# Kernel tuning notes

Measured on AMD Instinct MI355X. Metric: run time of the kernel, lower is better.

Reference implementation:

```python
import jax, jax.numpy as jnp
import numpy as np

D_MODEL = 1024
N_HEADS = 16
HEAD_DIM = 64
INNER = N_HEADS * HEAD_DIM
D_FF = 4096


def ln_novar(x, w, b):
    # mean-only 'layernorm' (no variance division), per original LayerNormNoVar
    u = jnp.mean(x, axis=-1, keepdims=True)
    return w * (x - u) + b


def setup_inputs() -> dict:
    key = jax.random.key(0)
    ks = jax.random.split(key, 12)
    s = lambda k, shape, scale: jax.random.normal(k, shape, dtype=jnp.float32) * scale
    inp = {
        "src": s(ks[0], (4, 2048, D_MODEL), 1.0),
        "pre_norm_w": jnp.ones((D_MODEL,), jnp.float32),
        "pre_norm_b": jnp.zeros((D_MODEL,), jnp.float32),
        "wq": s(ks[1], (D_MODEL, INNER), 0.02),
        "wk": s(ks[2], (D_MODEL, INNER), 0.02),
        "wv": s(ks[3], (D_MODEL, INNER), 0.02),
        "w_proj": s(ks[4], (INNER, D_MODEL), 0.02),
        "b_proj": jnp.zeros((D_MODEL,), jnp.float32),
        "norm1_w": jnp.ones((D_MODEL,), jnp.float32),
        "norm1_b": jnp.zeros((D_MODEL,), jnp.float32),
        "w1": s(ks[5], (D_MODEL, D_FF), 0.02),
        "b1": jnp.zeros((D_FF,), jnp.float32),
        "w2": s(ks[6], (D_FF, D_MODEL), 0.02),
        "b2": jnp.zeros((D_MODEL,), jnp.float32),
    }
    return inp


def reference(src, pre_norm_w, pre_norm_b, wq, wk, wv, w_proj, b_proj,
              norm1_w, norm1_b, w1, b1, w2, b2):
    B, N, _ = src.shape
    scale = HEAD_DIM ** -0.5
    x = ln_novar(src, pre_norm_w, pre_norm_b)
    q = (x @ wq).reshape(B, N, N_HEADS, HEAD_DIM)
    k = (x @ wk).reshape(B, N, N_HEADS, HEAD_DIM)
    v = (x @ wv).reshape(B, N, N_HEADS, HEAD_DIM)
    attn = jnp.einsum('bqhd,bkhd->bhqk', q, k) * scale
    attn = jax.nn.softmax(attn, axis=-1)
    o = jnp.einsum('bhqk,bkhd->bqhd', attn, v).reshape(B, N, INNER)
    o = o @ w_proj + b_proj
    src = src + o
    src = ln_novar(src, norm1_w, norm1_b)
    ff = jax.nn.relu(src @ w1 + b1) @ w2 + b2
    return src + ff
```

## Files before the change

### kernel.cpp

```cpp
#include <hip/hip_runtime.h>
#include <hip/hip_bf16.h>
#include <stdint.h>

typedef __hip_bfloat16 bf16;
typedef float f32x4 __attribute__((ext_vector_type(4)));
typedef float f32x16 __attribute__((ext_vector_type(16)));
typedef short v8s __attribute__((ext_vector_type(8)));
typedef __bf16 v8bf __attribute__((ext_vector_type(8)));
typedef unsigned int v4u __attribute__((ext_vector_type(4)));
typedef unsigned int u32;

static constexpr int MROWS = 8192;
static constexpr int DM    = 1024;
static constexpr int DFF   = 4096;
static constexpr int SEQ   = 2048;

__device__ __forceinline__ f32x4 mfma16(v8s a, v8s b, f32x4 c) {
  return __builtin_amdgcn_mfma_f32_16x16x32_bf16(
      __builtin_bit_cast(v8bf, a), __builtin_bit_cast(v8bf, b), c, 0, 0, 0);
}
__device__ __forceinline__ f32x16 mfma32(v8s a, v8s b, f32x16 c) {
  return __builtin_amdgcn_mfma_f32_32x32x16_bf16(
      __builtin_bit_cast(v8bf, a), __builtin_bit_cast(v8bf, b), c, 0, 0, 0);
}

__device__ __forceinline__ void gload_lds16(const void* g, void* l) {
  __builtin_amdgcn_global_load_lds(
      (const __attribute__((address_space(1))) void*)g,
      (__attribute__((address_space(3))) void*)l, 16, 0, 0);
}

__device__ __forceinline__ u32 cvtpk_bf16(float a, float b) {
  u32 r;
  asm("v_cvt_pk_bf16_f32 %0, %1, %2" : "=v"(r) : "v"(a), "v"(b));
  return r;
}
__device__ __forceinline__ void pl32swap(u32& x, u32& y) {
  asm volatile("v_permlane32_swap_b32 %0, %1" : "+v"(x), "+v"(y));
}
__device__ __forceinline__ float fast_exp2(float x) {
  float r;
  asm("v_exp_f32 %0, %1" : "=v"(r) : "v"(x));
  return r;
}

__global__ __launch_bounds__(256) void transpose_cast(
    const float* __restrict__ W, bf16* __restrict__ WT, int K, int N) {
  __shared__ float tile[32][33];
  const int c0 = blockIdx.x * 32;
  const int r0 = blockIdx.y * 32;
  const int tx = threadIdx.x & 31, ty = threadIdx.x >> 5;
  #pragma unroll
  for (int i = 0; i < 32; i += 8)
    tile[ty + i][tx] = W[(size_t)(r0 + ty + i) * N + c0 + tx];
  __syncthreads();
  #pragma unroll
  for (int i = 0; i < 32; i += 8)
    WT[(size_t)(c0 + ty + i) * K + r0 + tx] = __float2bfloat16(tile[tx][ty + i]);
}

__global__ __launch_bounds__(256) void ln_novar_kernel(
    const float* __restrict__ x, const float* __restrict__ w,
    const float* __restrict__ b, bf16* __restrict__ ob, float* __restrict__ of) {
  const int row = blockIdx.x;
  const int t = threadIdx.x;
  const float4 v = ((const float4*)(x + (size_t)row * DM))[t];
  float s = v.x + v.y + v.z + v.w;
  #pragma unroll
  for (int off = 32; off > 0; off >>= 1) s += __shfl_down(s, off, 64);
  __shared__ float wsum[4];
  if ((t & 63) == 0) wsum[t >> 6] = s;
  __syncthreads();
  const float u = (wsum[0] + wsum[1] + wsum[2] + wsum[3]) * (1.0f / DM);
  const float4 wv = ((const float4*)w)[t];
  const float4 bv = ((const float4*)b)[t];
  const float o0 = wv.x * (v.x - u) + bv.x;
  const float o1 = wv.y * (v.y - u) + bv.y;
  const float o2 = wv.z * (v.z - u) + bv.z;
  const float o3 = wv.w * (v.w - u) + bv.w;
  bf16* op = ob + (size_t)row * DM + t * 4;
  op[0] = __float2bfloat16(o0); op[1] = __float2bfloat16(o1);
  op[2] = __float2bfloat16(o2); op[3] = __float2bfloat16(o3);
  if (of) {
    float4 o4; o4.x = o0; o4.y = o1; o4.z = o2; o4.w = o3;
    ((float4*)(of + (size_t)row * DM))[t] = o4;
  }
}

#define BM 256
#define BN 128
#define BK 64
#define ASZ (BM * BK)
#define BSZ (BN * BK)
template <int EPI>
__global__ __launch_bounds__(512) void gemm_bt(
    const bf16* __restrict__ A, const bf16* __restrict__ BT,
    bf16* __restrict__ Cb, float* __restrict__ Cf,
    const float* __restrict__ bias, const float* __restrict__ res,
    int M, int Nn, int K) {
  __shared__ __align__(16) bf16 S[3][ASZ + BSZ];

  const int tid = threadIdx.x;
  const int lane = tid & 63;
  const int wave = tid >> 6;
  const int wr = wave >> 1, wc = wave & 1;

  const int nwg = gridDim.x;
  const int nbx = Nn / BN;
  int bid = (blockIdx.x & 7) * (nwg >> 3) + (blockIdx.x >> 3);
  const int GM = 4;
  const int grp = bid / (GM * nbx);
  const int rem = bid - grp * (GM * nbx);
  const int by = grp * GM + (rem & (GM - 1));
  const int bx = rem >> 2;
  const int tM = by * BM, tN = bx * BN;

  f32x4 acc[4][4] = {};
  const int nk = K / BK;

  auto STAGE = [&](int buf, int kt) {
    const int k0 = kt * BK;
    bf16* Ab = &S[buf][0];
    bf16* Bb = &S[buf][ASZ];
    #pragma unroll
    for (int c = 0; c < 4; ++c) {
      const int slot = c * 512 + tid;
      const int row = slot >> 3, s = slot & 7;
      const int kk = ((s ^ (row & 7)) << 3);
      gload_lds16(A + (size_t)(tM + row) * K + k0 + kk, (void*)(Ab + slot * 8));
    }
    #pragma unroll
    for (int c = 0; c < 2; ++c) {
      const int slot = c * 512 + tid;
      const int row = slot >> 3, s = slot & 7;
      const int kk = ((s ^ (row & 7)) << 3);
      gload_lds16(BT + (size_t)(tN + row) * K + k0 + kk, (void*)(Bb + slot * 8));
    }
  };

  STAGE(0, 0);
  STAGE(1, 1);

  for (int kt = 0; kt < nk; ++kt) {
    const int cur = kt % 3;
    if (kt + 2 < nk) STAGE((kt + 2) % 3, kt + 2);

    if (kt + 2 < nk)      asm volatile("s_waitcnt vmcnt(12)" ::: "memory");
    else if (kt + 1 < nk) asm volatile("s_waitcnt vmcnt(6)" ::: "memory");
    else                  asm volatile("s_waitcnt vmcnt(0)" ::: "memory");
    __builtin_amdgcn_s_barrier();
    asm volatile("" ::: "memory");

    const bf16* Ab = &S[cur][0];
    const bf16* Bb = &S[cur][ASZ];
    #pragma unroll
    for (int kk = 0; kk < 2; ++kk) {
      const int kslot = kk * 4 + (lane >> 4);
      v8s af[4], bfr[4];
      #pragma unroll
      for (int m = 0; m < 4; ++m) {
        const int row = wr * 64 + m * 16 + (lane & 15);
        af[m] = *(const v8s*)(Ab + (row * 8 + (kslot ^ (row & 7))) * 8);
      }
      #pragma unroll
      for (int n = 0; n < 4; ++n) {
        const int row = wc * 64 + n * 16 + (lane & 15);
        bfr[n] = *(const v8s*)(Bb + (row * 8 + (kslot ^ (row & 7))) * 8);
      }
      __builtin_amdgcn_s_setprio(1);
      #pragma unroll
      for (int m = 0; m < 4; ++m)
        #pragma unroll
        for (int n = 0; n < 4; ++n)
          acc[m][n] = mfma16(af[m], bfr[n], acc[m][n]);
      __builtin_amdgcn_s_setprio(0);
    }

    asm volatile("" ::: "memory");
    __builtin_amdgcn_s_barrier();
    asm volatile("" ::: "memory");
  }

  #pragma unroll
  for (int m = 0; m < 4; ++m) {
    #pragma unroll
    for (int n = 0; n < 4; ++n) {
      const int row0 = tM + wr * 64 + m * 16 + ((lane >> 4) << 2);
      const int col = tN + wc * 64 + n * 16 + (lane & 15);
      #pragma unroll
      for (int r = 0; r < 4; ++r) {
        const size_t idx = (size_t)(row0 + r) * Nn + col;
        float v = acc[m][n][r];
        if (EPI == 0) {
          Cb[idx] = __float2bfloat16(v);
        } else if (EPI == 1) {
          v += bias[col];
          v = fmaxf(v, 0.0f);
          Cb[idx] = __float2bfloat16(v);
        } else {
          v += bias[col] + res[idx];
          Cf[idx] = v;
        }
      }
    }
  }
}

__global__ __launch_bounds__(256) void repack_kv(
    const bf16* __restrict__ qkv, bf16* __restrict__ krep,
    bf16* __restrict__ vrep) {
  const int bhkt = blockIdx.x;
  const int bh = bhkt >> 5, kt = bhkt & 31;
  const int b = bh >> 4, h = bh & 15;
  const size_t obase = (size_t)bhkt * 4096;
  #pragma unroll
  for (int it = 0; it < 16; ++it) {
    const int o = it * 256 + threadIdx.x;
    const int ch = o >> 9, rowi = (o >> 3) & 63, e = o & 7;
    krep[obase + o] =
        qkv[(size_t)(b * SEQ + kt * 64 + rowi) * 3072 + 1024 + h * 64 + ch * 8 + e];
    vrep[obase + o] =
        qkv[(size_t)(b * SEQ + kt * 64 + ch * 8 + e) * 3072 + 2048 + h * 64 + rowi];
  }
}

#define PPV(i) ((i) < 16 ? s0[(i) & 15] : s1[(i) & 15])
__global__ __launch_bounds__(256, 4) void attn_kernel(
    const bf16* __restrict__ qkv, const bf16* __restrict__ krep,
    const bf16* __restrict__ vrep, bf16* __restrict__ ob) {
  const int qt = blockIdx.x & 15;
  const int bh = blockIdx.x >> 4;
  const int b = bh >> 4, h = bh & 15;
  const int tid = threadIdx.x;
  const int lane = tid & 63, wave = tid >> 6;
  const int c = lane & 31, hi = lane >> 5;
  const float CEXP = 0.180336880111120426f;

  __shared__ __align__(16) bf16 Ks[2][4096];
  __shared__ __align__(16) bf16 Vs[2][4096];

  const int qrow = qt * 128 + wave * 32 + c;
  const bf16* qp = qkv + (size_t)(b * SEQ + qrow) * 3072 + h * 64;
  v8s qf[4];
  #pragma unroll
  for (int ks = 0; ks < 4; ++ks)
    qf[ks] = *(const v8s*)(qp + ks * 16 + hi * 8);

  f32x16 o0 = {}, o1 = {};
  float mrow = -1e30f, lrow = 0.0f;

  const size_t tilebase = (size_t)(bh * 32) * 4096;
  #pragma unroll
  for (int j = 0; j < 2; ++j) {
    gload_lds16(krep + tilebase + (tid + j * 256) * 8, &Ks[0][(tid + j * 256) * 8]);
    gload_lds16(vrep + tilebase + (tid + j * 256) * 8, &Vs[0][(tid + j * 256) * 8]);
  }
  asm volatile("s_waitcnt vmcnt(0)" ::: "memory");
  __builtin_amdgcn_s_barrier();
  asm volatile("" ::: "memory");

  for (int kt = 0; kt < 32; ++kt) {
    const int cur = kt & 1;
    if (kt < 31) {
      const size_t nb = tilebase + (size_t)(kt + 1) * 4096;
      #pragma unroll
      for (int j = 0; j < 2; ++j) {
        gload_lds16(krep + nb + (tid + j * 256) * 8, &Ks[cur ^ 1][(tid + j * 256) * 8]);
        gload_lds16(vrep + nb + (tid + j * 256) * 8, &Vs[cur ^ 1][(tid + j * 256) * 8]);
      }
    }
    const bf16* KB = Ks[cur];
    const bf16* VB = Vs[cur];

    f32x16 s0 = {}, s1 = {};
    __builtin_amdgcn_s_setprio(1);
    #pragma unroll
    for (int ks = 0; ks < 4; ++ks) {
      const int ch = (2 * ks + hi) * 512;
      v8s a0 = *(const v8s*)(KB + ch + c * 8);
      v8s a1 = *(const v8s*)(KB + ch + (c + 32) * 8);
      s0 = mfma32(a0, qf[ks], s0);
      s1 = mfma32(a1, qf[ks], s1);
    }
    __builtin_amdgcn_s_setprio(0);

    float mA = -1e30f, mB = -1e30f;
    #pragma unroll
    for (int i = 0; i < 16; i += 2) {
      mA = fmaxf(fmaxf(s0[i], s0[i + 1]), mA);
      mB = fmaxf(fmaxf(s1[i], s1[i + 1]), mB);
    }
    float tmax = fmaxf(mA, mB);
    tmax = fmaxf(tmax, __shfl_xor(tmax, 32, 64));
    if (__any(tmax - mrow > 64.0f)) {
      const float mnew = fmaxf(mrow, tmax);
      const float ef = fast_exp2((mrow - mnew) * CEXP);
      mrow = mnew;
      lrow *= ef;
      #pragma unroll
      for (int r = 0; r < 16; ++r) {
        const float efq = __shfl(ef, (r & 3) + 8 * (r >> 2) + 4 * hi, 64);
        o0[r] *= efq;
        o1[r] *= efq;
      }
    }
    const float nmc = -mrow * CEXP;
    float rs0 = 0.0f, rs1 = 0.0f;
    #pragma unroll
    for (int i = 0; i < 16; ++i) {
      s0[i] = fast_exp2(fmaf(s0[i], CEXP, nmc));
      s1[i] = fast_exp2(fmaf(s1[i], CEXP, nmc));
      rs0 += s0[i];
      rs1 += s1[i];
    }
    float rs = rs0 + rs1;
    rs += __shfl_xor(rs, 32, 64);
    lrow += rs;

    v8s pa[4];
    #pragma unroll
    for (int ks = 0; ks < 4; ++ks) {
      u32 x  = cvtpk_bf16(PPV(8 * ks + 0), PPV(8 * ks + 1));
      u32 y  = cvtpk_bf16(PPV(8 * ks + 4), PPV(8 * ks + 5));
      u32 x2 = cvtpk_bf16(PPV(8 * ks + 2), PPV(8 * ks + 3));
      u32 y2 = cvtpk_bf16(PPV(8 * ks + 6), PPV(8 * ks + 7));
      pl32swap(x, y);
      pl32swap(x2, y2);
      v4u w; w.x = x; w.y = x2; w.z = y; w.w = y2;
      pa[ks] = __builtin_bit_cast(v8s, w);
    }

    __builtin_amdgcn_s_setprio(1);
    #pragma unroll
    for (int ks = 0; ks < 4; ++ks) {
      const int ch = (2 * ks + hi) * 512;
      v8s b0 = *(const v8s*)(VB + ch + c * 8);
      v8s b1 = *(const v8s*)(VB + ch + (c + 32) * 8);
      o0 = mfma32(pa[ks], b0, o0);
      o1 = mfma32(pa[ks], b1, o1);
    }
    __builtin_amdgcn_s_setprio(0);

    asm volatile("s_waitcnt vmcnt(0)" ::: "memory");
    __builtin_amdgcn_s_barrier();
    asm volatile("" ::: "memory");
  }

  const float rl = 1.0f / lrow;
  const size_t orow0 = (size_t)(b * SEQ + qt * 128 + wave * 32);
  #pragma unroll
  for (int r = 0; r < 16; ++r) {
    const int q = (r & 3) + 8 * (r >> 2) + 4 * hi;
    const float rq = __shfl(rl, q, 64);
    bf16* op = ob + (orow0 + q) * DM + h * 64;
    op[c] = __float2bfloat16(o0[r] * rq);
    op[32 + c] = __float2bfloat16(o1[r] * rq);
  }
}

extern "C" void kernel_launch(void* const* d_in, const int* in_sizes, int n_in,
                              void* d_out, int out_size, void* d_ws,
                              size_t ws_size, hipStream_t stream) {
  const float* src   = (const float*)d_in[0];
  const float* pnw   = (const float*)d_in[1];
  const float* pnb   = (const float*)d_in[2];
  const float* wq    = (const float*)d_in[3];
  const float* wk    = (const float*)d_in[4];
  const float* wv    = (const float*)d_in[5];
  const float* wproj = (const float*)d_in[6];
  const float* bproj = (const float*)d_in[7];
  const float* n1w   = (const float*)d_in[8];
  const float* n1b   = (const float*)d_in[9];
  const float* w1    = (const float*)d_in[10];
  const float* b1    = (const float*)d_in[11];
  const float* w2    = (const float*)d_in[12];
  const float* b2    = (const float*)d_in[13];
  float* out = (float*)d_out;

  char* ws = (char*)d_ws;
  size_t off = 0;
  bf16* WTqkv = (bf16*)(ws + off); off += (size_t)3072 * 1024 * 2;
  bf16* WTprj = (bf16*)(ws + off); off += (size_t)1024 * 1024 * 2;
  bf16* WT1   = (bf16*)(ws + off); off += (size_t)4096 * 1024 * 2;
  bf16* WT2   = (bf16*)(ws + off); off += (size_t)1024 * 4096 * 2;
  bf16* xb    = (bf16*)(ws + off); off += (size_t)MROWS * DM * 2;
  bf16* qkvb  = (bf16*)(ws + off); off += (size_t)MROWS * 3072 * 2;
  bf16* obuf  = (bf16*)(ws + off); off += (size_t)MROWS * DM * 2;
  float* yf   = (float*)(ws + off); off += (size_t)MROWS * DM * 4;
  bf16* h1    = (bf16*)(ws + off); off += (size_t)MROWS * DFF * 2;
  bf16* krep = h1;
  bf16* vrep = h1 + (size_t)64 * SEQ * 64;

  const dim3 blk(256);
  const dim3 gblk(512);

  transpose_cast<<<dim3(32, 32), blk, 0, stream>>>(wq, WTqkv, 1024, 1024);
  transpose_cast<<<dim3(32, 32), blk, 0, stream>>>(wk, WTqkv + 1024 * 1024, 1024, 1024);
  transpose_cast<<<dim3(32, 32), blk, 0, stream>>>(wv, WTqkv + 2048 * 1024, 1024, 1024);
  transpose_cast<<<dim3(32, 32), blk, 0, stream>>>(wproj, WTprj, 1024, 1024);
  transpose_cast<<<dim3(128, 32), blk, 0, stream>>>(w1, WT1, 1024, 4096);
  transpose_cast<<<dim3(32, 128), blk, 0, stream>>>(w2, WT2, 4096, 1024);

  ln_novar_kernel<<<MROWS, blk, 0, stream>>>(src, pnw, pnb, xb, nullptr);

  gemm_bt<0><<<dim3((3072 / BN) * (MROWS / BM)), gblk, 0, stream>>>(
      xb, WTqkv, qkvb, nullptr, nullptr, nullptr, MROWS, 3072, 1024);

  repack_kv<<<dim3(64 * 32), blk, 0, stream>>>(qkvb, krep, vrep);

  attn_kernel<<<dim3(16 * 64), dim3(256), 0, stream>>>(qkvb, krep, vrep, obuf);

  gemm_bt<2><<<dim3((1024 / BN) * (MROWS / BM)), gblk, 0, stream>>>(
      obuf, WTprj, nullptr, yf, bproj, src, MROWS, 1024, 1024);

  ln_novar_kernel<<<MROWS, blk, 0, stream>>>(yf, n1w, n1b, xb, out);

  gemm_bt<1><<<dim3((4096 / BN) * (MROWS / BM)), gblk, 0, stream>>>(
      xb, WT1, h1, nullptr, b1, nullptr, MROWS, 4096, 1024);

  gemm_bt<2><<<dim3((1024 / BN) * (MROWS / BM)), gblk, 0, stream>>>(
      h1, WT2, nullptr, out, b2, out, MROWS, 1024, 4096);
}
```

Before: 428.6 us.

## Transpose GEMM tile to 128x256 and interleave half-stage loads with MFMA phases

The GEMM block tile becomes 128x256 with a 2x4 wave grid instead of 256x128 with 4x2. Prefetch of stage kt+2 is split into two halves, issued after the LDS fragment reads of each k-subslice. Barriers now sit around each subslice's MFMA block, with a reworked vmcnt schedule and a prologue wait. The aim is to spread global-to-LDS traffic across the compute phases and cut the per-iteration stall at the top of the loop, at the cost of extra barriers per k-tile. The grid mapping still uses the old swizzle, which assumed the old tile shape.

After: 432.7 us. No clear change (+0.9%).

```diff
diff --git a/kernel.cpp b/kernel.cpp
--- a/kernel.cpp
+++ b/kernel.cpp
@@ -87,8 +87,8 @@
   }
 }
 
-#define BM 256
-#define BN 128
+#define BM 128
+#define BN 256
 #define BK 64
 #define ASZ (BM * BK)
 #define BSZ (BN * BK)
@@ -103,7 +103,8 @@
   const int tid = threadIdx.x;
   const int lane = tid & 63;
   const int wave = tid >> 6;
-  const int wr = wave >> 1, wc = wave & 1;
+  const int wr = wave >> 2;
+  const int wcn = wave & 3;
 
   const int nwg = gridDim.x;
   const int nbx = Nn / BN;
@@ -118,39 +119,33 @@
   f32x4 acc[4][4] = {};
   const int nk = K / BK;
 
-  auto STAGE = [&](int buf, int kt) {
+  auto STAGE_H = [&](int buf, int kt, int hf) {
     const int k0 = kt * BK;
     bf16* Ab = &S[buf][0];
     bf16* Bb = &S[buf][ASZ];
-    #pragma unroll
-    for (int c = 0; c < 4; ++c) {
-      const int slot = c * 512 + tid;
+    {
+      const int slot = hf * 512 + tid;
       const int row = slot >> 3, s = slot & 7;
       const int kk = ((s ^ (row & 7)) << 3);
       gload_lds16(A + (size_t)(tM + row) * K + k0 + kk, (void*)(Ab + slot * 8));
     }
     #pragma unroll
-    for (int c = 0; c < 2; ++c) {
-      const int slot = c * 512 + tid;
+    for (int c2 = 0; c2 < 2; ++c2) {
+      const int slot = hf * 1024 + c2 * 512 + tid;
       const int row = slot >> 3, s = slot & 7;
       const int kk = ((s ^ (row & 7)) << 3);
       gload_lds16(BT + (size_t)(tN + row) * K + k0 + kk, (void*)(Bb + slot * 8));
     }
   };
 
-  STAGE(0, 0);
-  STAGE(1, 1);
+  STAGE_H(0, 0, 0); STAGE_H(0, 0, 1);
+  STAGE_H(1, 1, 0); STAGE_H(1, 1, 1);
+  asm volatile("s_waitcnt vmcnt(6)" ::: "memory");
+  __builtin_amdgcn_s_barrier();
+  asm volatile("" ::: "memory");
 
   for (int kt = 0; kt < nk; ++kt) {
     const int cur = kt % 3;
-    if (kt + 2 < nk) STAGE((kt + 2) % 3, kt + 2);
-
-    if (kt + 2 < nk)      asm volatile("s_waitcnt vmcnt(12)" ::: "memory");
-    else if (kt + 1 < nk) asm volatile("s_waitcnt vmcnt(6)" ::: "memory");
-    else                  asm volatile("s_waitcnt vmcnt(0)" ::: "memory");
-    __builtin_amdgcn_s_barrier();
-    asm volatile("" ::: "memory");
-
     const bf16* Ab = &S[cur][0];
     const bf16* Bb = &S[cur][ASZ];
     #pragma unroll
@@ -164,9 +159,16 @@
       }
       #pragma unroll
       for (int n = 0; n < 4; ++n) {
-        const int row = wc * 64 + n * 16 + (lane & 15);
+        const int row = wcn * 64 + n * 16 + (lane & 15);
         bfr[n] = *(const v8s*)(Bb + (row * 8 + (kslot ^ (row & 7))) * 8);
       }
+      if (kt + 2 < nk) STAGE_H((kt + 2) % 3, kt + 2, kk);
+      if (kk == 1) {
+        if (kt + 2 < nk) asm volatile("s_waitcnt vmcnt(6)" ::: "memory");
+        else             asm volatile("s_waitcnt vmcnt(0)" ::: "memory");
+      }
+      __builtin_amdgcn_s_barrier();
+      asm volatile("" ::: "memory");
       __builtin_amdgcn_s_setprio(1);
       #pragma unroll
       for (int m = 0; m < 4; ++m)
@@ -174,11 +176,10 @@
         for (int n = 0; n < 4; ++n)
           acc[m][n] = mfma16(af[m], bfr[n], acc[m][n]);
       __builtin_amdgcn_s_setprio(0);
-    }
-
-    asm volatile("" ::: "memory");
-    __builtin_amdgcn_s_barrier();
-    asm volatile("" ::: "memory");
+      asm volatile("" ::: "memory");
+      __builtin_amdgcn_s_barrier();
+      asm volatile("" ::: "memory");
+    }
   }
 
   #pragma unroll
@@ -186,7 +187,7 @@
     #pragma unroll
     for (int n = 0; n < 4; ++n) {
       const int row0 = tM + wr * 64 + m * 16 + ((lane >> 4) << 2);
-      const int col = tN + wc * 64 + n * 16 + (lane & 15);
+      const int col = tN + wcn * 64 + n * 16 + (lane & 15);
       #pragma unroll
       for (int r = 0; r < 4; ++r) {
         const size_t idx = (size_t)(row0 + r) * Nn + col;
```
